# Optimization experiments

Hardware: AMD Instinct MI355X
Metric: run time of the kernel (lower is better)

The kernel has to match this reference:

```python
import jax, jax.numpy as jnp
import numpy as np

HID = 1024
NH = 16
HD = 64
INTER = 2816
EPS = 1e-5


def _rms_norm(x, eps=EPS):
    x32 = x.astype(jnp.float32)
    var = jnp.mean(x32 * x32, axis=-1, keepdims=True)
    return (x32 * jax.lax.rsqrt(var + eps)).astype(x.dtype)


def _rotate_half(x):
    x1, x2 = jnp.split(x, 2, axis=-1)
    return jnp.concatenate([-x2, x1], axis=-1)


def setup_inputs() -> dict:
    key = jax.random.key(0)
    ks = jax.random.split(key, 6)
    B, S = 1, 2048
    # real RoPE tables: [S, HD]
    inv_freq = 1.0 / (10000.0 ** (np.arange(0, HD, 2, dtype=np.float32) / HD))
    t = np.arange(S, dtype=np.float32)
    freqs = np.outer(t, inv_freq)  # [S, HD/2]
    emb = np.concatenate([freqs, freqs], axis=-1)  # [S, HD]
    cos = jnp.asarray(np.cos(emb))
    sin = jnp.asarray(np.sin(emb))
    sc = 0.02
    return {
        "cos": cos,
        "sin": sin,
        "hidden_states": jax.random.normal(ks[0], (B, S, HID), jnp.float32),
        "attn_bias": jax.random.normal(ks[1], (B, NH, S, S), jnp.float32) * 0.1,
        "w_qkv": jax.random.normal(ks[2], (HID, (NH + 2 * NH) * HD), jnp.float32) * sc,
        "w_o": jax.random.normal(ks[3], (NH * HD, HID), jnp.float32) * sc,
        "w_gate_up": jax.random.normal(ks[4], (HID, 2 * INTER), jnp.float32) * sc,
        "w_down": jax.random.normal(ks[5], (INTER, HID), jnp.float32) * sc,
    }


def _attention(cos, sin, x, attn_bias, w_qkv, w_o):
    B, S, _ = x.shape
    qkv = (x @ w_qkv).reshape(B, S, 3 * NH, HD)
    q = qkv[:, :, :NH]          # [B,S,H,D]
    k = qkv[:, :, NH:2 * NH]
    v = qkv[:, :, 2 * NH:]
    c = cos[None, :, None, :]
    s = sin[None, :, None, :]
    q = q * c + _rotate_half(q) * s
    k = k * c + _rotate_half(k) * s
    scale = HD ** -0.5
    scores = jnp.einsum('bqhd,bkhd->bhqk', q, k) * scale + attn_bias
    attn = jax.nn.softmax(scores.astype(jnp.float32), axis=-1).astype(q.dtype)
    out = jnp.einsum('bhqk,bkhd->bqhd', attn, v).reshape(B, S, NH * HD)
    return out @ w_o


def _swiglu(x, w_gate_up, w_down):
    gu = x @ w_gate_up
    gate, up = jnp.split(gu, 2, axis=-1)
    return (jax.nn.silu(gate) * up) @ w_down


def reference(cos, sin, hidden_states, attn_bias, w_qkv, w_o, w_gate_up, w_down):
    x = hidden_states
    x = _rms_norm(x + _attention(cos, sin, x, attn_bias, w_qkv, w_o))
    x = _rms_norm(x + _swiglu(x, w_gate_up, w_down))
    return x
```

## Files before the change

### kernel.cpp

```cpp
#include <hip/hip_runtime.h>
#include <stdint.h>

using u16 = unsigned short;
typedef __bf16 bf16x8 __attribute__((ext_vector_type(8)));
typedef float f32x4 __attribute__((ext_vector_type(4)));

__device__ __forceinline__ u16 f2bf(float f) {
  union { float f; uint32_t u; } v; v.f = f;
  uint32_t r = v.u + 0x7fffu + ((v.u >> 16) & 1u);
  return (u16)(r >> 16);
}
__device__ __forceinline__ float bf2f(u16 h) {
  union { uint32_t u; float f; } v; v.u = ((uint32_t)h) << 16;
  return v.f;
}
__device__ __forceinline__ bf16x8 ldb8(const u16* p) {
  return *reinterpret_cast<const bf16x8*>(p);
}
__device__ __forceinline__ void gload_lds16(const void* g, void* l) {
  __builtin_amdgcn_global_load_lds(
      (const __attribute__((address_space(1))) void*)g,
      (__attribute__((address_space(3))) void*)l, 16, 0, 0);
}

__global__ __launch_bounds__(256) void prep_kernel(
    const float* __restrict__ w_qkv, const float* __restrict__ w_o,
    const float* __restrict__ w_gu, const float* __restrict__ w_down,
    const float* __restrict__ hidden, u16* __restrict__ wqkv_t,
    u16* __restrict__ wo_t, u16* __restrict__ wgu_t, u16* __restrict__ wd_t,
    u16* __restrict__ xb) {
  const int b = blockIdx.x;
  const int t = threadIdx.x;

  if (b >= 12544) {
    int idx = (b - 12544) * 256 + t;
    float4 v = *(const float4*)(hidden + (size_t)idx * 4);
    ushort4 o;
    o.x = f2bf(v.x); o.y = f2bf(v.y); o.z = f2bf(v.z); o.w = f2bf(v.w);
    *(ushort4*)(xb + (size_t)idx * 4) = o;
    return;
  }

  const float* W;
  u16* Wt;
  int N, K, lb;
  bool perm = false;
  if (b < 3072)      { W = w_qkv; Wt = wqkv_t; N = 3072; K = 1024; lb = b; }
  else if (b < 4096) { W = w_o;   Wt = wo_t;   N = 1024; K = 1024; lb = b - 3072; }
  else if (b < 9728) { W = w_gu;  Wt = wgu_t;  N = 5632; K = 1024; lb = b - 4096; perm = true; }
  else               { W = w_down; Wt = wd_t;  N = 1024; K = 2816; lb = b - 9728; }

  const int nx = N >> 5;
  const int n0 = (lb % nx) * 32, k0 = (lb / nx) * 32;
  const int tx = t & 31, ty = t >> 5;

  __shared__ u16 tile[32][33];
  const int nc = n0 + tx;
  const int src_col = perm ? (((nc & 1) == 0) ? (nc >> 1) : 2816 + (nc >> 1))
                           : nc;
#pragma unroll
  for (int i = 0; i < 32; i += 8)
    tile[ty + i][tx] = f2bf(W[(size_t)(k0 + ty + i) * N + src_col]);
  __syncthreads();
#pragma unroll
  for (int i = 0; i < 32; i += 8)
    Wt[(size_t)(n0 + ty + i) * K + k0 + tx] = tile[tx][ty + i];
}

__global__ __launch_bounds__(256) void gemm_qkv_rope(
    const u16* __restrict__ A, const u16* __restrict__ Bt,
    const float* __restrict__ cosb, const float* __restrict__ sinb,
    u16* __restrict__ qb, u16* __restrict__ kb, u16* __restrict__ vt,
    int M, int N, int K) {
  __shared__ __align__(16) u16 As[128 * 32];
  __shared__ __align__(16) u16 Bs[128 * 32];
  __shared__ u16 vbuf[4][64][17];
  const int tid = threadIdx.x;
  const int w = tid >> 6, lane = tid & 63;
  const int wr = w >> 1, wc = w & 1;
  const int r16 = lane & 15, g = lane >> 4;
  const int nwg = gridDim.x * gridDim.y;
  const int idx = blockIdx.y * gridDim.x + blockIdx.x;
  const int swz = (idx & 7) * (nwg >> 3) + (idx >> 3);
  const int m0 = (swz / gridDim.x) * 128, n0 = (swz % gridDim.x) * 128;
  const int ldrow = lane >> 2;
  const int ldk = (lane & 3) * 8;

  f32x4 acc[4][4] = {};

  for (int kt = 0; kt < K; kt += 32) {
#pragma unroll
    for (int i = 0; i < 2; ++i) {
      int chunk = w * 2 + i;
      int row = chunk * 16 + ldrow;
      gload_lds16(A + (size_t)(m0 + row) * K + kt + ldk, &As[chunk * 512]);
      gload_lds16(Bt + (size_t)(n0 + row) * K + kt + ldk, &Bs[chunk * 512]);
    }
    __syncthreads();
    bf16x8 a[4], b[4];
#pragma unroll
    for (int mt = 0; mt < 4; ++mt)
      a[mt] = ldb8(&As[(wr * 64 + mt * 16 + r16) * 32 + g * 8]);
#pragma unroll
    for (int nt = 0; nt < 4; ++nt)
      b[nt] = ldb8(&Bs[(wc * 64 + nt * 16 + r16) * 32 + g * 8]);
#pragma unroll
    for (int mt = 0; mt < 4; ++mt)
#pragma unroll
      for (int nt = 0; nt < 4; ++nt)
        acc[mt][nt] = __builtin_amdgcn_mfma_f32_16x16x32_bf16(
            a[mt], b[nt], acc[mt][nt], 0, 0, 0);
    __syncthreads();
  }

  const int type = n0 >> 10;
  const int head = ((n0 & 1023) >> 6) + wc;
  if (type < 2) {
    u16* outp = type == 0 ? qb : kb;
    const float qs = type == 0 ? 0.125f : 1.0f;
#pragma unroll
    for (int mt = 0; mt < 4; ++mt)
#pragma unroll
      for (int r = 0; r < 4; ++r) {
        const int srow = m0 + wr * 64 + mt * 16 + g * 4 + r;
#pragma unroll
        for (int nt = 0; nt < 4; ++nt) {
          const int d = nt * 16 + r16;
          float cv = cosb[srow * 64 + d];
          float sv = sinb[srow * 64 + d];
          float sgn = nt < 2 ? -1.f : 1.f;
          float val = acc[mt][nt][r] * cv + sgn * acc[mt][nt ^ 2][r] * sv;
          outp[((size_t)head * 2048 + srow) * 64 + d] = f2bf(val * qs);
        }
      }
  } else {
    const int s_base = m0 + wr * 64;
    const int dl = lane >> 2;
    const int sblk = (lane & 3) * 16;
#pragma unroll
    for (int nt = 0; nt < 4; ++nt) {
#pragma unroll
      for (int mt = 0; mt < 4; ++mt)
#pragma unroll
        for (int r = 0; r < 4; ++r)
          vbuf[w][mt * 16 + g * 4 + r][r16] = f2bf(acc[mt][nt][r]);
      u16* dst =
          vt + ((size_t)(head * 64 + nt * 16 + dl)) * 2048 + s_base + sblk;
#pragma unroll
      for (int jj = 0; jj < 4; ++jj) {
        ushort4 ov;
        ov.x = vbuf[w][sblk + jj * 4 + 0][dl];
        ov.y = vbuf[w][sblk + jj * 4 + 1][dl];
        ov.z = vbuf[w][sblk + jj * 4 + 2][dl];
        ov.w = vbuf[w][sblk + jj * 4 + 3][dl];
        *(ushort4*)(dst + jj * 4) = ov;
      }
    }
  }
}

__global__ __launch_bounds__(256) void gemm_bt_swiglu(
    const u16* __restrict__ A, const u16* __restrict__ Bt,
    u16* __restrict__ Hb, int M, int N, int K) {
  __shared__ __align__(16) u16 As[128 * 32];
  __shared__ __align__(16) u16 Bs[128 * 32];
  const int tid = threadIdx.x;
  const int w = tid >> 6, lane = tid & 63;
  const int wr = w >> 1, wc = w & 1;
  const int r16 = lane & 15, g = lane >> 4;
  const int nwg = gridDim.x * gridDim.y;
  const int idx = blockIdx.y * gridDim.x + blockIdx.x;
  const int swz = (idx & 7) * (nwg >> 3) + (idx >> 3);
  const int m0 = (swz / gridDim.x) * 128, n0 = (swz % gridDim.x) * 128;
  const int ldrow = lane >> 2;
  const int ldk = (lane & 3) * 8;

  f32x4 acc[4][4] = {};

  for (int kt = 0; kt < K; kt += 32) {
#pragma unroll
    for (int i = 0; i < 2; ++i) {
      int chunk = w * 2 + i;
      int row = chunk * 16 + ldrow;
      gload_lds16(A + (size_t)(m0 + row) * K + kt + ldk, &As[chunk * 512]);
      gload_lds16(Bt + (size_t)(n0 + row) * K + kt + ldk, &Bs[chunk * 512]);
    }
    __syncthreads();
    bf16x8 a[4], b[4];
#pragma unroll
    for (int mt = 0; mt < 4; ++mt)
      a[mt] = ldb8(&As[(wr * 64 + mt * 16 + r16) * 32 + g * 8]);
#pragma unroll
    for (int nt = 0; nt < 4; ++nt)
      b[nt] = ldb8(&Bs[(wc * 64 + nt * 16 + r16) * 32 + g * 8]);
#pragma unroll
    for (int mt = 0; mt < 4; ++mt)
#pragma unroll
      for (int nt = 0; nt < 4; ++nt)
        acc[mt][nt] = __builtin_amdgcn_mfma_f32_16x16x32_bf16(
            a[mt], b[nt], acc[mt][nt], 0, 0, 0);
    __syncthreads();
  }
#pragma unroll
  for (int mt = 0; mt < 4; ++mt)
#pragma unroll
    for (int nt = 0; nt < 4; ++nt)
#pragma unroll
      for (int r = 0; r < 4; ++r) {
        float val = acc[mt][nt][r];
        float other = __shfl_xor(val, 1);
        if ((r16 & 1) == 0) {
          float o = val / (1.f + __expf(-val)) * other;
          int row = m0 + wr * 64 + mt * 16 + g * 4 + r;
          int col = n0 + wc * 64 + nt * 16 + r16;
          Hb[(size_t)row * 2816 + (col >> 1)] = f2bf(o);
        }
      }
}

__global__ __launch_bounds__(256) void gemm_bt6464(
    const u16* __restrict__ A, const u16* __restrict__ Bt,
    u16* __restrict__ C, int M, int N, int K) {
  __shared__ __align__(16) u16 As[64 * 32];
  __shared__ __align__(16) u16 Bs[64 * 32];
  const int tid = threadIdx.x;
  const int w = tid >> 6, lane = tid & 63;
  const int wr = w >> 1, wc = w & 1;
  const int r16 = lane & 15, g = lane >> 4;
  const int nwg = gridDim.x * gridDim.y;
  const int idx = blockIdx.y * gridDim.x + blockIdx.x;
  const int swz = (idx & 7) * (nwg >> 3) + (idx >> 3);
  const int m0 = (swz / gridDim.x) * 64, n0 = (swz % gridDim.x) * 64;
  const int ldrow = lane >> 2;
  const int ldk = (lane & 3) * 8;

  f32x4 acc[2][2] = {};

  for (int kt = 0; kt < K; kt += 32) {
#pragma unroll
    for (int i = 0; i < 2; ++i) {
      int chunk = w * 2 + i;
      if (chunk < 4) {
        int row = chunk * 16 + ldrow;
        gload_lds16(A + (size_t)(m0 + row) * K + kt + ldk, &As[chunk * 512]);
      } else {
        int cb = chunk - 4;
        int row = cb * 16 + ldrow;
        gload_lds16(Bt + (size_t)(n0 + row) * K + kt + ldk, &Bs[cb * 512]);
      }
    }
    __syncthreads();
    bf16x8 a[2], b[2];
#pragma unroll
    for (int mt = 0; mt < 2; ++mt)
      a[mt] = ldb8(&As[(wr * 32 + mt * 16 + r16) * 32 + g * 8]);
#pragma unroll
    for (int nt = 0; nt < 2; ++nt)
      b[nt] = ldb8(&Bs[(wc * 32 + nt * 16 + r16) * 32 + g * 8]);
#pragma unroll
    for (int mt = 0; mt < 2; ++mt)
#pragma unroll
      for (int nt = 0; nt < 2; ++nt)
        acc[mt][nt] = __builtin_amdgcn_mfma_f32_16x16x32_bf16(
            a[mt], b[nt], acc[mt][nt], 0, 0, 0);
    __syncthreads();
  }
#pragma unroll
  for (int mt = 0; mt < 2; ++mt)
#pragma unroll
    for (int nt = 0; nt < 2; ++nt)
#pragma unroll
      for (int r = 0; r < 4; ++r) {
        int row = m0 + wr * 32 + mt * 16 + g * 4 + r;
        int col = n0 + wc * 32 + nt * 16 + r16;
        C[(size_t)row * N + col] = f2bf(acc[mt][nt][r]);
      }
}

__global__ __launch_bounds__(256, 2) void attn_kernel(
    const u16* __restrict__ qb, const u16* __restrict__ kb,
    const u16* __restrict__ vt, const float* __restrict__ bias,
    u16* __restrict__ attnb) {
  const int bid = blockIdx.x;
  const int swz = (bid & 7) * 64 + (bid >> 3);
  const int h = swz >> 5;
  const int qt = swz & 31;
  const int tid = threadIdx.x;
  const int w = tid >> 6;
  const int lane = tid & 63;
  const int r16 = lane & 15, g = lane >> 4;

  __shared__ __align__(16) u16 P_lds[4][16 * 40];
  __shared__ float acc_s[4][16][64];
  __shared__ float m_s[4][16], l_s[4][16];

  bf16x8 qf0[4], qf1[4];
#pragma unroll
  for (int st = 0; st < 4; ++st) {
    const u16* qrow =
        qb + ((size_t)h * 2048 + qt * 64 + st * 16 + r16) * 64;
    qf0[st] = ldb8(qrow + g * 8);
    qf1[st] = ldb8(qrow + 32 + g * 8);
  }

  f32x4 acc[4][4] = {};
  float m[4], lsum[4];
#pragma unroll
  for (int st = 0; st < 4; ++st) { m[st] = -1e30f; lsum[st] = 0.f; }

  const float* bbase = bias + ((size_t)h * 2048 + qt * 64) * 2048;

  const int kv0 = w * 512, kv1 = kv0 + 512;
  for (int kt = kv0; kt < kv1; kt += 32) {
    bf16x8 ka[2], kc[2];
#pragma unroll
    for (int c = 0; c < 2; ++c) {
      const u16* krow = kb + ((size_t)h * 2048 + kt + c * 16 + r16) * 64;
      ka[c] = ldb8(krow + g * 8);
      kc[c] = ldb8(krow + 32 + g * 8);
    }
    bf16x8 vf[4];
#pragma unroll
    for (int nt = 0; nt < 4; ++nt)
      vf[nt] =
          ldb8(vt + ((size_t)h * 64 + nt * 16 + r16) * 2048 + kt + g * 8);

#pragma unroll
    for (int st = 0; st < 4; ++st) {
      float4 bv0 = *(const float4*)(bbase +
          (size_t)(st * 16 + r16) * 2048 + kt + g * 4);
      float4 bv1 = *(const float4*)(bbase +
          (size_t)(st * 16 + r16) * 2048 + kt + 16 + g * 4);

      f32x4 sc[2];
#pragma unroll
      for (int c = 0; c < 2; ++c) {
        f32x4 z = {0.f, 0.f, 0.f, 0.f};
        f32x4 t =
            __builtin_amdgcn_mfma_f32_16x16x32_bf16(ka[c], qf0[st], z, 0, 0, 0);
        sc[c] =
            __builtin_amdgcn_mfma_f32_16x16x32_bf16(kc[c], qf1[st], t, 0, 0, 0);
      }
      sc[0][0] += bv0.x; sc[0][1] += bv0.y; sc[0][2] += bv0.z; sc[0][3] += bv0.w;
      sc[1][0] += bv1.x; sc[1][1] += bv1.y; sc[1][2] += bv1.z; sc[1][3] += bv1.w;

      float t8 = fmaxf(fmaxf(fmaxf(sc[0][0], sc[0][1]), fmaxf(sc[0][2], sc[0][3])),
                       fmaxf(fmaxf(sc[1][0], sc[1][1]), fmaxf(sc[1][2], sc[1][3])));
      t8 = fmaxf(t8, __shfl_xor(t8, 16));
      t8 = fmaxf(t8, __shfl_xor(t8, 32));
      float mnew = fmaxf(m[st], t8);
      float alpha = __expf(m[st] - mnew);
      m[st] = mnew;

      float ps = 0.f;
#pragma unroll
      for (int c = 0; c < 2; ++c)
#pragma unroll
        for (int r = 0; r < 4; ++r) {
          float p = __expf(sc[c][r] - mnew);
          sc[c][r] = p;
          ps += p;
        }
      lsum[st] = lsum[st] * alpha + ps;

      float av[4];
#pragma unroll
      for (int r = 0; r < 4; ++r) av[r] = __shfl(alpha, g * 4 + r);
#pragma unroll
      for (int nt = 0; nt < 4; ++nt)
#pragma unroll
        for (int r = 0; r < 4; ++r) acc[st][nt][r] *= av[r];

#pragma unroll
      for (int c = 0; c < 2; ++c)
#pragma unroll
        for (int r = 0; r < 4; ++r)
          P_lds[w][r16 * 40 + c * 16 + g * 4 + r] = f2bf(sc[c][r]);
      bf16x8 pf = ldb8(&P_lds[w][r16 * 40 + g * 8]);
#pragma unroll
      for (int nt = 0; nt < 4; ++nt)
        acc[st][nt] = __builtin_amdgcn_mfma_f32_16x16x32_bf16(
            pf, vf[nt], acc[st][nt], 0, 0, 0);
    }
  }

#pragma unroll
  for (int st = 0; st < 4; ++st) {
    __syncthreads();
#pragma unroll
    for (int nt = 0; nt < 4; ++nt)
#pragma unroll
      for (int r = 0; r < 4; ++r)
        acc_s[w][g * 4 + r][nt * 16 + r16] = acc[st][nt][r];
    {
      float t = lsum[st];
      t += __shfl_xor(t, 16);
      t += __shfl_xor(t, 32);
      if (lane < 16) {
        l_s[w][r16] = t;
        m_s[w][r16] = m[st];
      }
    }
    __syncthreads();

    const int row = tid >> 4;
    const int col4 = (tid & 15) * 4;
    float m0v = m_s[0][row], m1v = m_s[1][row], m2v = m_s[2][row],
          m3v = m_s[3][row];
    float mm = fmaxf(fmaxf(m0v, m1v), fmaxf(m2v, m3v));
    float s0 = __expf(m0v - mm), s1 = __expf(m1v - mm);
    float s2 = __expf(m2v - mm), s3 = __expf(m3v - mm);
    float ltot = l_s[0][row] * s0 + l_s[1][row] * s1 + l_s[2][row] * s2 +
                 l_s[3][row] * s3;
    float inv = 1.f / ltot;
    ushort4 ov;
    u16* outp =
        attnb + (size_t)(qt * 64 + st * 16 + row) * 1024 + h * 64 + col4;
#pragma unroll
    for (int j = 0; j < 4; ++j) {
      float v = acc_s[0][row][col4 + j] * s0 + acc_s[1][row][col4 + j] * s1 +
                acc_s[2][row][col4 + j] * s2 + acc_s[3][row][col4 + j] * s3;
      ((u16*)&ov)[j] = f2bf(v * inv);
    }
    *(ushort4*)outp = ov;
  }
}

__global__ __launch_bounds__(256) void addnorm_kernel(
    const float* __restrict__ resid, const u16* __restrict__ delta,
    float* __restrict__ outf, u16* __restrict__ outb) {
  int row = blockIdx.x, tid = threadIdx.x;
  size_t base = (size_t)row * 1024 + tid * 4;
  float4 rv = *(const float4*)(resid + base);
  ushort4 dv = *(const ushort4*)(delta + base);
  float x0 = rv.x + bf2f(dv.x);
  float x1 = rv.y + bf2f(dv.y);
  float x2 = rv.z + bf2f(dv.z);
  float x3 = rv.w + bf2f(dv.w);
  float ss = x0 * x0 + x1 * x1 + x2 * x2 + x3 * x3;
#pragma unroll
  for (int sh = 32; sh >= 1; sh >>= 1) ss += __shfl_xor(ss, sh);
  __shared__ float red[4];
  if ((tid & 63) == 0) red[tid >> 6] = ss;
  __syncthreads();
  float tot = red[0] + red[1] + red[2] + red[3];
  float rstd = rsqrtf(tot * (1.0f / 1024.0f) + 1e-5f);
  float4 ov;
  ov.x = x0 * rstd; ov.y = x1 * rstd; ov.z = x2 * rstd; ov.w = x3 * rstd;
  *(float4*)(outf + base) = ov;
  if (outb) {
    ushort4 ob;
    ob.x = f2bf(ov.x); ob.y = f2bf(ov.y); ob.z = f2bf(ov.z); ob.w = f2bf(ov.w);
    *(ushort4*)(outb + base) = ob;
  }
}

extern "C" void kernel_launch(void* const* d_in, const int* in_sizes, int n_in,
                              void* d_out, int out_size, void* d_ws,
                              size_t ws_size, hipStream_t stream) {
  (void)in_sizes; (void)n_in; (void)out_size; (void)ws_size;
  const float* cosb  = (const float*)d_in[0];
  const float* sinb  = (const float*)d_in[1];
  const float* hidden = (const float*)d_in[2];
  const float* bias  = (const float*)d_in[3];
  const float* w_qkv = (const float*)d_in[4];
  const float* w_o   = (const float*)d_in[5];
  const float* w_gu  = (const float*)d_in[6];
  const float* w_down = (const float*)d_in[7];
  float* out = (float*)d_out;

  char* p = (char*)d_ws;
  auto alloc = [&](size_t bytes) {
    void* r = (void*)p;
    p += (bytes + 255) & ~(size_t)255;
    return r;
  };
  u16* wqkv_t = (u16*)alloc((size_t)3072 * 1024 * 2);
  u16* wo_t   = (u16*)alloc((size_t)1024 * 1024 * 2);
  u16* wgu_t  = (u16*)alloc((size_t)5632 * 1024 * 2);
  u16* wd_t   = (u16*)alloc((size_t)1024 * 2816 * 2);
  u16* xb     = (u16*)alloc((size_t)2048 * 1024 * 2);
  u16* qb     = (u16*)alloc((size_t)16 * 2048 * 64 * 2);
  u16* kb     = (u16*)alloc((size_t)16 * 2048 * 64 * 2);
  u16* vt     = (u16*)alloc((size_t)16 * 2048 * 64 * 2);
  u16* attnb  = (u16*)alloc((size_t)2048 * 1024 * 2);
  u16* ob     = (u16*)alloc((size_t)2048 * 1024 * 2);
  float* x1f  = (float*)alloc((size_t)2048 * 1024 * 4);
  u16* x1b    = (u16*)alloc((size_t)2048 * 1024 * 2);
  u16* hb     = (u16*)alloc((size_t)2048 * 2816 * 2);
  u16* mlpb   = (u16*)alloc((size_t)2048 * 1024 * 2);

  prep_kernel<<<14592, 256, 0, stream>>>(w_qkv, w_o, w_gu, w_down, hidden,
                                         wqkv_t, wo_t, wgu_t, wd_t, xb);

  gemm_qkv_rope<<<dim3(3072 / 128, 2048 / 128), 256, 0, stream>>>(
      xb, wqkv_t, cosb, sinb, qb, kb, vt, 2048, 3072, 1024);
  attn_kernel<<<512, 256, 0, stream>>>(qb, kb, vt, bias, attnb);
  gemm_bt6464<<<dim3(1024 / 64, 2048 / 64), 256, 0, stream>>>(attnb, wo_t, ob, 2048, 1024, 1024);
  addnorm_kernel<<<2048, 256, 0, stream>>>(hidden, ob, x1f, x1b);
  gemm_bt_swiglu<<<dim3(5632 / 128, 2048 / 128), 256, 0, stream>>>(x1b, wgu_t, hb, 2048, 5632, 1024);
  gemm_bt6464<<<dim3(1024 / 64, 2048 / 64), 256, 0, stream>>>(hb, wd_t, mlpb, 2048, 1024, 2816);
  addnorm_kernel<<<2048, 256, 0, stream>>>(x1f, mlpb, out, nullptr);
}
```

Baseline: 249.7 us.

## Double-buffer LDS tiles in GEMM kernels to overlap global loads with MFMA

Converts the three GEMM kernels (QKV+RoPE, gate/up SwiGLU, 64x64 generic) from single-buffered LDS staging to a ping-pong double buffer. The next K-tile is issued via global_load_lds before the current tile's MFMAs run, and the two barriers per iteration become one explicit waitcnt plus barrier. This is meant to hide global memory latency behind matrix math. It doubles LDS use per block, which can lower occupancy, and the waitcnt still stalls on the prefetch at the end of each iteration.

```diff
diff --git a/kernel.cpp b/kernel.cpp
--- a/kernel.cpp
+++ b/kernel.cpp
@@ -72,8 +72,8 @@
     const float* __restrict__ cosb, const float* __restrict__ sinb,
     u16* __restrict__ qb, u16* __restrict__ kb, u16* __restrict__ vt,
     int M, int N, int K) {
-  __shared__ __align__(16) u16 As[128 * 32];
-  __shared__ __align__(16) u16 Bs[128 * 32];
+  __shared__ __align__(16) u16 As[2][128 * 32];
+  __shared__ __align__(16) u16 Bs[2][128 * 32];
   __shared__ u16 vbuf[4][64][17];
   const int tid = threadIdx.x;
   const int w = tid >> 6, lane = tid & 63;
@@ -85,32 +85,46 @@
   const int m0 = (swz / gridDim.x) * 128, n0 = (swz % gridDim.x) * 128;
   const int ldrow = lane >> 2;
   const int ldk = (lane & 3) * 8;
+  const int NT = K >> 5;
 
   f32x4 acc[4][4] = {};
 
-  for (int kt = 0; kt < K; kt += 32) {
-#pragma unroll
-    for (int i = 0; i < 2; ++i) {
-      int chunk = w * 2 + i;
-      int row = chunk * 16 + ldrow;
-      gload_lds16(A + (size_t)(m0 + row) * K + kt + ldk, &As[chunk * 512]);
-      gload_lds16(Bt + (size_t)(n0 + row) * K + kt + ldk, &Bs[chunk * 512]);
-    }
-    __syncthreads();
+#define STG_QKV(tt, b_)                                                   \
+  do {                                                                    \
+    const int kt_ = (tt) * 32;                                            \
+    _Pragma("unroll") for (int i = 0; i < 2; ++i) {                       \
+      int chunk = w * 2 + i;                                              \
+      int row = chunk * 16 + ldrow;                                       \
+      gload_lds16(A + (size_t)(m0 + row) * K + kt_ + ldk,                 \
+                  &As[b_][chunk * 512]);                                  \
+      gload_lds16(Bt + (size_t)(n0 + row) * K + kt_ + ldk,                \
+                  &Bs[b_][chunk * 512]);                                  \
+    }                                                                     \
+  } while (0)
+
+  STG_QKV(0, 0);
+  asm volatile("s_waitcnt vmcnt(0)" ::: "memory");
+  __builtin_amdgcn_s_barrier();
+
+  int cur = 0;
+  for (int t = 0; t < NT; ++t) {
+    if (t + 1 < NT) STG_QKV(t + 1, cur ^ 1);
     bf16x8 a[4], b[4];
 #pragma unroll
     for (int mt = 0; mt < 4; ++mt)
-      a[mt] = ldb8(&As[(wr * 64 + mt * 16 + r16) * 32 + g * 8]);
+      a[mt] = ldb8(&As[cur][(wr * 64 + mt * 16 + r16) * 32 + g * 8]);
 #pragma unroll
     for (int nt = 0; nt < 4; ++nt)
-      b[nt] = ldb8(&Bs[(wc * 64 + nt * 16 + r16) * 32 + g * 8]);
+      b[nt] = ldb8(&Bs[cur][(wc * 64 + nt * 16 + r16) * 32 + g * 8]);
 #pragma unroll
     for (int mt = 0; mt < 4; ++mt)
 #pragma unroll
       for (int nt = 0; nt < 4; ++nt)
         acc[mt][nt] = __builtin_amdgcn_mfma_f32_16x16x32_bf16(
             a[mt], b[nt], acc[mt][nt], 0, 0, 0);
-    __syncthreads();
+    asm volatile("s_waitcnt vmcnt(0) lgkmcnt(0)" ::: "memory");
+    __builtin_amdgcn_s_barrier();
+    cur ^= 1;
   }
 
   const int type = n0 >> 10;
@@ -162,8 +176,8 @@
 __global__ __launch_bounds__(256) void gemm_bt_swiglu(
     const u16* __restrict__ A, const u16* __restrict__ Bt,
     u16* __restrict__ Hb, int M, int N, int K) {
-  __shared__ __align__(16) u16 As[128 * 32];
-  __shared__ __align__(16) u16 Bs[128 * 32];
+  __shared__ __align__(16) u16 As[2][128 * 32];
+  __shared__ __align__(16) u16 Bs[2][128 * 32];
   const int tid = threadIdx.x;
   const int w = tid >> 6, lane = tid & 63;
   const int wr = w >> 1, wc = w & 1;
@@ -174,32 +188,33 @@
   const int m0 = (swz / gridDim.x) * 128, n0 = (swz % gridDim.x) * 128;
   const int ldrow = lane >> 2;
   const int ldk = (lane & 3) * 8;
+  const int NT = K >> 5;
 
   f32x4 acc[4][4] = {};
 
-  for (int kt = 0; kt < K; kt += 32) {
-#pragma unroll
-    for (int i = 0; i < 2; ++i) {
-      int chunk = w * 2 + i;
-      int row = chunk * 16 + ldrow;
-      gload_lds16(A + (size_t)(m0 + row) * K + kt + ldk, &As[chunk * 512]);
-      gload_lds16(Bt + (size_t)(n0 + row) * K + kt + ldk, &Bs[chunk * 512]);
-    }
-    __syncthreads();
+  STG_QKV(0, 0);
+  asm volatile("s_waitcnt vmcnt(0)" ::: "memory");
+  __builtin_amdgcn_s_barrier();
+
+  int cur = 0;
+  for (int t = 0; t < NT; ++t) {
+    if (t + 1 < NT) STG_QKV(t + 1, cur ^ 1);
     bf16x8 a[4], b[4];
 #pragma unroll
     for (int mt = 0; mt < 4; ++mt)
-      a[mt] = ldb8(&As[(wr * 64 + mt * 16 + r16) * 32 + g * 8]);
+      a[mt] = ldb8(&As[cur][(wr * 64 + mt * 16 + r16) * 32 + g * 8]);
 #pragma unroll
     for (int nt = 0; nt < 4; ++nt)
-      b[nt] = ldb8(&Bs[(wc * 64 + nt * 16 + r16) * 32 + g * 8]);
+      b[nt] = ldb8(&Bs[cur][(wc * 64 + nt * 16 + r16) * 32 + g * 8]);
 #pragma unroll
     for (int mt = 0; mt < 4; ++mt)
 #pragma unroll
       for (int nt = 0; nt < 4; ++nt)
         acc[mt][nt] = __builtin_amdgcn_mfma_f32_16x16x32_bf16(
             a[mt], b[nt], acc[mt][nt], 0, 0, 0);
-    __syncthreads();
+    asm volatile("s_waitcnt vmcnt(0) lgkmcnt(0)" ::: "memory");
+    __builtin_amdgcn_s_barrier();
+    cur ^= 1;
   }
 #pragma unroll
   for (int mt = 0; mt < 4; ++mt)
@@ -221,8 +236,8 @@
 __global__ __launch_bounds__(256) void gemm_bt6464(
     const u16* __restrict__ A, const u16* __restrict__ Bt,
     u16* __restrict__ C, int M, int N, int K) {
-  __shared__ __align__(16) u16 As[64 * 32];
-  __shared__ __align__(16) u16 Bs[64 * 32];
+  __shared__ __align__(16) u16 As[2][64 * 32];
+  __shared__ __align__(16) u16 Bs[2][64 * 32];
   const int tid = threadIdx.x;
   const int w = tid >> 6, lane = tid & 63;
   const int wr = w >> 1, wc = w & 1;
@@ -233,37 +248,51 @@
   const int m0 = (swz / gridDim.x) * 64, n0 = (swz % gridDim.x) * 64;
   const int ldrow = lane >> 2;
   const int ldk = (lane & 3) * 8;
+  const int NT = K >> 5;
 
   f32x4 acc[2][2] = {};
 
-  for (int kt = 0; kt < K; kt += 32) {
-#pragma unroll
-    for (int i = 0; i < 2; ++i) {
-      int chunk = w * 2 + i;
-      if (chunk < 4) {
-        int row = chunk * 16 + ldrow;
-        gload_lds16(A + (size_t)(m0 + row) * K + kt + ldk, &As[chunk * 512]);
-      } else {
-        int cb = chunk - 4;
-        int row = cb * 16 + ldrow;
-        gload_lds16(Bt + (size_t)(n0 + row) * K + kt + ldk, &Bs[cb * 512]);
-      }
-    }
-    __syncthreads();
+#define STG_6464(tt, b_)                                                  \
+  do {                                                                    \
+    const int kt_ = (tt) * 32;                                            \
+    _Pragma("unroll") for (int i = 0; i < 2; ++i) {                       \
+      int chunk = w * 2 + i;                                              \
+      if (chunk < 4) {                                                    \
+        int row = chunk * 16 + ldrow;                                     \
+        gload_lds16(A + (size_t)(m0 + row) * K + kt_ + ldk,               \
+                    &As[b_][chunk * 512]);                                \
+      } else {                                                            \
+        int cb = chunk - 4;                                               \
+        int row = cb * 16 + ldrow;                                        \
+        gload_lds16(Bt + (size_t)(n0 + row) * K + kt_ + ldk,              \
+                    &Bs[b_][cb * 512]);                                   \
+      }                                                                   \
+    }                                                                     \
+  } while (0)
+
+  STG_6464(0, 0);
+  asm volatile("s_waitcnt vmcnt(0)" ::: "memory");
+  __builtin_amdgcn_s_barrier();
+
+  int cur = 0;
+  for (int t = 0; t < NT; ++t) {
+    if (t + 1 < NT) STG_6464(t + 1, cur ^ 1);
     bf16x8 a[2], b[2];
 #pragma unroll
     for (int mt = 0; mt < 2; ++mt)
-      a[mt] = ldb8(&As[(wr * 32 + mt * 16 + r16) * 32 + g * 8]);
+      a[mt] = ldb8(&As[cur][(wr * 32 + mt * 16 + r16) * 32 + g * 8]);
 #pragma unroll
     for (int nt = 0; nt < 2; ++nt)
-      b[nt] = ldb8(&Bs[(wc * 32 + nt * 16 + r16) * 32 + g * 8]);
+      b[nt] = ldb8(&Bs[cur][(wc * 32 + nt * 16 + r16) * 32 + g * 8]);
 #pragma unroll
     for (int mt = 0; mt < 2; ++mt)
 #pragma unroll
       for (int nt = 0; nt < 2; ++nt)
         acc[mt][nt] = __builtin_amdgcn_mfma_f32_16x16x32_bf16(
             a[mt], b[nt], acc[mt][nt], 0, 0, 0);
-    __syncthreads();
+    asm volatile("s_waitcnt vmcnt(0) lgkmcnt(0)" ::: "memory");
+    __builtin_amdgcn_s_barrier();
+    cur ^= 1;
   }
 #pragma unroll
   for (int mt = 0; mt < 2; ++mt)
```

Measured after the change: 242.3 us. -3.0%, faster.
